# Performance work log

Hardware: AMD Instinct MI355X
Metric: run time of the kernel (lower is better)

## Reference

```python
import jax, jax.numpy as jnp
import numpy as np
from jax import lax

EPS = 1e-5
NUM_GROUPS = 32
OFFSET_SCALE = 1.0
K = 3            # deformable conv kernel size
KK = K * K
DWK = 7          # depthwise kernel size for offset predictor


def group_norm(x, gamma, beta, num_groups=NUM_GROUPS):
    B, C, H, W = x.shape
    xg = x.reshape(B, num_groups, C // num_groups, H, W)
    m = xg.mean(axis=(2, 3, 4), keepdims=True)
    v = xg.var(axis=(2, 3, 4), keepdims=True)
    xn = ((xg - m) * lax.rsqrt(v + EPS)).reshape(B, C, H, W)
    return xn * gamma[None, :, None, None] + beta[None, :, None, None]


def bilinear_gather(x, py, px):
    # x: [B,C,H,W]; py, px: [B,KK,H,W] absolute sample coords -> [B,C,KK,H,W]
    B, C, H, W = x.shape
    y0 = jnp.floor(py)
    x0 = jnp.floor(px)
    wy1 = py - y0
    wx1 = px - x0
    wy0 = 1.0 - wy1
    wx0 = 1.0 - wx1
    xf = x.reshape(B, C, H * W)

    def gather(yi, xi):
        valid = (yi >= 0) & (yi <= H - 1) & (xi >= 0) & (xi <= W - 1)
        yc = jnp.clip(yi, 0, H - 1).astype(jnp.int32)
        xc = jnp.clip(xi, 0, W - 1).astype(jnp.int32)
        idx = (yc * W + xc).reshape(B, -1)                      # [B, KK*H*W]
        g = jax.vmap(lambda a, i: a[:, i])(xf, idx)             # [B, C, KK*H*W]
        g = g.reshape(B, C, KK, H, W)
        return g * valid.astype(x.dtype)[:, None]

    out = (gather(y0, x0) * (wy0 * wx0)[:, None]
           + gather(y0, x0 + 1.0) * (wy0 * wx1)[:, None]
           + gather(y0 + 1.0, x0) * (wy1 * wx0)[:, None]
           + gather(y0 + 1.0, x0 + 1.0) * (wy1 * wx1)[:, None])
    return out


def deform_conv(x, dw, pw, pwb, w, b):
    # x: [B,C,H,W]; dw: [C,1,DWK,DWK] depthwise; pw: [2*KK,C,1,1]; w: [O,C,K,K]
    B, C, H, W = x.shape
    dn = ('NCHW', 'OIHW', 'NCHW')
    f = lax.conv_general_dilated(x, dw, (1, 1), 'SAME',
                                 feature_group_count=C, dimension_numbers=dn)
    off = lax.conv_general_dilated(f, pw, (1, 1), 'SAME', dimension_numbers=dn)
    off = (off + pwb[None, :, None, None]) * OFFSET_SCALE       # [B,2*KK,H,W]
    off = off.reshape(B, KK, 2, H, W)
    ks = jnp.arange(K, dtype=x.dtype) - (K - 1) / 2             # [-1,0,1]
    ky = jnp.repeat(ks, K)                                      # [KK]
    kx = jnp.tile(ks, K)
    yy, xx = jnp.meshgrid(jnp.arange(H, dtype=x.dtype),
                          jnp.arange(W, dtype=x.dtype), indexing='ij')
    py = yy[None, None] + ky[None, :, None, None] + off[:, :, 0]  # [B,KK,H,W]
    px = xx[None, None] + kx[None, :, None, None] + off[:, :, 1]
    sampled = bilinear_gather(x, py, px)                        # [B,C,KK,H,W]
    O = w.shape[0]
    out = jnp.einsum('bckhw,ock->bohw', sampled, w.reshape(O, C, KK))
    return out + b[None, :, None, None]


def setup_inputs() -> dict:
    key = jax.random.key(0)
    ks = jax.random.split(key, 10)
    B, C, H, W = 4, 256, 64, 64
    O = C
    x = jax.random.normal(ks[0], (B, C, H, W), dtype=jnp.float32)

    def conv_w(k, shape, fan_in):
        return jax.random.normal(k, shape, dtype=jnp.float32) / np.sqrt(fan_in)

    inp = {
        'x': x,
        'gn1_g': jnp.ones((C,), jnp.float32), 'gn1_b': jnp.zeros((C,), jnp.float32),
        'dw1': conv_w(ks[1], (C, 1, DWK, DWK), DWK * DWK),
        'pw1': jax.random.normal(ks[2], (2 * KK, C, 1, 1), jnp.float32) * 0.01,
        'pwb1': jnp.zeros((2 * KK,), jnp.float32),
        'w1': conv_w(ks[3], (O, C, K, K), C * KK),
        'b1': jnp.zeros((O,), jnp.float32),
        'gn2_g': jnp.ones((O,), jnp.float32), 'gn2_b': jnp.zeros((O,), jnp.float32),
        'dw2': conv_w(ks[4], (O, 1, DWK, DWK), DWK * DWK),
        'pw2': jax.random.normal(ks[5], (2 * KK, O, 1, 1), jnp.float32) * 0.01,
        'pwb2': jnp.zeros((2 * KK,), jnp.float32),
        'w2': conv_w(ks[6], (O, O, K, K), O * KK),
        'b2': jnp.zeros((O,), jnp.float32),
    }
    return inp


def reference(x, gn1_g, gn1_b, dw1, pw1, pwb1, w1, b1,
              gn2_g, gn2_b, dw2, pw2, pwb2, w2, b2):
    h = jax.nn.relu(group_norm(x, gn1_g, gn1_b))
    h = deform_conv(h, dw1, pw1, pwb1, w1, b1)
    h = jax.nn.relu(group_norm(h, gn2_g, gn2_b))
    # Dropout / DropPath are identity in eval mode
    h = deform_conv(h, dw2, pw2, pwb2, w2, b2)
    return h + x  # shortcut is Identity (in_channels == out_channels)
```

## Files before the change

### kernel.cpp

```cpp
#include <hip/hip_runtime.h>

#define B_    4
#define C_    256
#define H_    64
#define W_    64
#define HW_   4096
#define NG_   32
#define CPG_  8
#define KK_   9
#define NOFF_ 18

typedef __attribute__((ext_vector_type(8))) short short8;
typedef __attribute__((ext_vector_type(4))) short short4v;
typedef __attribute__((ext_vector_type(4))) float floatx4;

static __device__ __forceinline__ short f2bf(float f) {
    union { float f; unsigned u; } v; v.f = f;
    unsigned r = v.u + 0x7fff + ((v.u >> 16) & 1);
    return (short)(r >> 16);
}
static __device__ __forceinline__ float bf2f(short s) {
    union { unsigned u; float f; } v;
    v.u = ((unsigned)(unsigned short)s) << 16;
    return v.f;
}

__global__ __launch_bounds__(1024) void gn_relu_f32_kernel(
    const float* __restrict__ in, const float* __restrict__ gamma,
    const float* __restrict__ beta, short* __restrict__ outb)
{
    int b = blockIdx.x >> 5;
    int g = blockIdx.x & 31;
    const int N = CPG_ * HW_;
    size_t base = ((size_t)(b * C_ + g * CPG_)) * HW_;
    const float4* in4 = (const float4*)(in + base);
    int t = threadIdx.x;

    float s = 0.f, ss = 0.f;
    for (int i = t; i < N / 4; i += 1024) {
        float4 v = in4[i];
        s  += v.x + v.y + v.z + v.w;
        ss += v.x * v.x + v.y * v.y + v.z * v.z + v.w * v.w;
    }
    #pragma unroll
    for (int off = 32; off > 0; off >>= 1) {
        s  += __shfl_down(s, off, 64);
        ss += __shfl_down(ss, off, 64);
    }
    __shared__ float red[32];
    __shared__ float sh_rs, sh_m;
    int wid = t >> 6;
    if ((t & 63) == 0) { red[wid] = s; red[16 + wid] = ss; }
    __syncthreads();
    if (t == 0) {
        float S = 0.f, SS = 0.f;
        #pragma unroll
        for (int i = 0; i < 16; ++i) { S += red[i]; SS += red[16 + i]; }
        float m = S / (float)N;
        float var = SS / (float)N - m * m;
        sh_rs = rsqrtf(var + 1e-5f);
        sh_m = m;
    }
    __syncthreads();
    float rs = sh_rs, m = sh_m;
    short4v* out4 = (short4v*)(outb + base);
    for (int i = t; i < N / 4; i += 1024) {
        int ch = g * CPG_ + (i >> 10);
        float ga = gamma[ch] * rs;
        float be = beta[ch] - m * ga;
        float4 v = in4[i];
        short4v o;
        o.x = f2bf(fmaxf(fmaf(v.x, ga, be), 0.f));
        o.y = f2bf(fmaxf(fmaf(v.y, ga, be), 0.f));
        o.z = f2bf(fmaxf(fmaf(v.z, ga, be), 0.f));
        o.w = f2bf(fmaxf(fmaf(v.w, ga, be), 0.f));
        out4[i] = o;
    }
}

__global__ __launch_bounds__(1024) void gn_relu_bf16_kernel(
    const short* __restrict__ in, const float* __restrict__ gamma,
    const float* __restrict__ beta, short* __restrict__ outb)
{
    int b = blockIdx.x >> 5;
    int g = blockIdx.x & 31;
    const int N = CPG_ * HW_;
    size_t base = ((size_t)(b * C_ + g * CPG_)) * HW_;
    const short4v* in4 = (const short4v*)(in + base);
    int t = threadIdx.x;

    float s = 0.f, ss = 0.f;
    for (int i = t; i < N / 4; i += 1024) {
        short4v sv = in4[i];
        float vx = bf2f(sv.x), vy = bf2f(sv.y), vz = bf2f(sv.z), vw = bf2f(sv.w);
        s  += vx + vy + vz + vw;
        ss += vx * vx + vy * vy + vz * vz + vw * vw;
    }
    #pragma unroll
    for (int off = 32; off > 0; off >>= 1) {
        s  += __shfl_down(s, off, 64);
        ss += __shfl_down(ss, off, 64);
    }
    __shared__ float red[32];
    __shared__ float sh_rs, sh_m;
    int wid = t >> 6;
    if ((t & 63) == 0) { red[wid] = s; red[16 + wid] = ss; }
    __syncthreads();
    if (t == 0) {
        float S = 0.f, SS = 0.f;
        #pragma unroll
        for (int i = 0; i < 16; ++i) { S += red[i]; SS += red[16 + i]; }
        float m = S / (float)N;
        float var = SS / (float)N - m * m;
        sh_rs = rsqrtf(var + 1e-5f);
        sh_m = m;
    }
    __syncthreads();
    float rs = sh_rs, m = sh_m;
    short4v* out4 = (short4v*)(outb + base);
    for (int i = t; i < N / 4; i += 1024) {
        int ch = g * CPG_ + (i >> 10);
        float ga = gamma[ch] * rs;
        float be = beta[ch] - m * ga;
        short4v sv = in4[i];
        short4v o;
        o.x = f2bf(fmaxf(fmaf(bf2f(sv.x), ga, be), 0.f));
        o.y = f2bf(fmaxf(fmaf(bf2f(sv.y), ga, be), 0.f));
        o.z = f2bf(fmaxf(fmaf(bf2f(sv.z), ga, be), 0.f));
        o.w = f2bf(fmaxf(fmaf(bf2f(sv.w), ga, be), 0.f));
        out4[i] = o;
    }
}

__global__ __launch_bounds__(256) void dw7_kernel(
    const short* __restrict__ in, const float* __restrict__ dwk,
    short* __restrict__ out)
{
    int plane = blockIdx.x;
    int c = plane & (C_ - 1);
    const short* src = in + (size_t)plane * HW_;
    short* dst = out + (size_t)plane * HW_;
    __shared__ float tile[70 * 72];
    __shared__ float wk[49];
    int t = threadIdx.x;
    if (t < 49) wk[t] = dwk[c * 49 + t];
    for (int i = t; i < 70 * 72; i += 256) tile[i] = 0.f;
    __syncthreads();
    const short4v* src4 = (const short4v*)src;
    for (int i = t; i < HW_ / 4; i += 256) {
        short4v v = src4[i];
        int y = i >> 4, x = (i & 15) * 4;
        float* tp = &tile[(y + 3) * 72 + (x + 3)];
        tp[0] = bf2f(v.x); tp[1] = bf2f(v.y);
        tp[2] = bf2f(v.z); tp[3] = bf2f(v.w);
    }
    __syncthreads();
    #pragma unroll
    for (int it = 0; it < 4; ++it) {
        int idx = it * 256 + t;
        int y = idx >> 4;
        int x0 = (idx & 15) * 4;
        float a0 = 0.f, a1 = 0.f, a2 = 0.f, a3 = 0.f;
        #pragma unroll
        for (int dy = 0; dy < 7; ++dy) {
            const float* tr = &tile[(y + dy) * 72 + x0];
            float4 ra = *(const float4*)tr;
            float4 rb = *(const float4*)(tr + 4);
            float4 rc = *(const float4*)(tr + 8);
            float r[12] = {ra.x, ra.y, ra.z, ra.w,
                           rb.x, rb.y, rb.z, rb.w,
                           rc.x, rc.y, rc.z, rc.w};
            const float* wr = &wk[dy * 7];
            #pragma unroll
            for (int dx = 0; dx < 7; ++dx) {
                float wv = wr[dx];
                a0 = fmaf(r[dx], wv, a0);
                a1 = fmaf(r[dx + 1], wv, a1);
                a2 = fmaf(r[dx + 2], wv, a2);
                a3 = fmaf(r[dx + 3], wv, a3);
            }
        }
        short4v o;
        o.x = f2bf(a0); o.y = f2bf(a1); o.z = f2bf(a2); o.w = f2bf(a3);
        *(short4v*)&dst[y * 64 + x0] = o;
    }
}

__global__ __launch_bounds__(256) void transpose2_kernel(
    const short* __restrict__ srcA, short* __restrict__ dstA,
    const short* __restrict__ srcB, short* __restrict__ dstB)
{
    int blk = blockIdx.x;
    const short* src = (blk < 256) ? srcA : srcB;
    short*       dst = (blk < 256) ? dstA : dstB;
    int q = blk & 255;
    int b = q >> 6;
    int px0 = (q & 63) * 64;
    __shared__ unsigned ltile[64 * 132];
    int t = threadIdx.x;
    const short* sb = src + (size_t)b * C_ * HW_;

    int pq4 = t & 15, cphi = t >> 4;
    #pragma unroll
    for (int i = 0; i < 8; ++i) {
        int cp = i * 16 + cphi;
        const short* r0 = sb + (size_t)(2 * cp) * HW_ + px0 + pq4 * 4;
        short4v lo = *(const short4v*)r0;
        short4v hi = *(const short4v*)(r0 + HW_);
        #pragma unroll
        for (int j = 0; j < 4; ++j) {
            int pl = pq4 * 4 + j;
            unsigned wrd = (unsigned)(unsigned short)lo[j]
                         | ((unsigned)(unsigned short)hi[j] << 16);
            ltile[pl * 132 + (cp ^ ((pl & 7) << 2))] = wrd;
        }
    }
    __syncthreads();

    int co = t & 31, ph = t >> 5;
    #pragma unroll
    for (int r = 0; r < 8; ++r) {
        int pl = r * 8 + ph;
        uint4 v = *(const uint4*)&ltile[pl * 132 + ((co * 4) ^ ((pl & 7) << 2))];
        *(uint4*)(dst + ((size_t)b * HW_ + px0 + pl) * C_ + co * 8) = v;
    }
}

__global__ __launch_bounds__(256) void wpack_all_kernel(
    const float* __restrict__ w1, const float* __restrict__ w2,
    const float* __restrict__ pw1, const float* __restrict__ pw2,
    short* __restrict__ wp1, short* __restrict__ wp2,
    short* __restrict__ ppk1, short* __restrict__ ppk2)
{
    int blk = blockIdx.x;
    if (blk < 4608) {
        const float* w = (blk < 2304) ? w1 : w2;
        short* wp = (blk < 2304) ? wp1 : wp2;
        int idx = (blk % 2304) * 256 + threadIdx.x;
        int j    = idx & 7;
        int lane = (idx >> 3) & 63;
        int ot   = (idx >> 9) & 15;
        int slab = idx >> 13;
        int k = slab >> 3, cc = slab & 7;
        int o = ot * 16 + (lane & 15);
        int c = cc * 32 + (lane >> 4) * 8 + j;
        wp[idx] = f2bf(w[(size_t)(o * C_ + c) * KK_ + k]);
    } else {
        int q = blk - 4608;
        const float* pw = (q < 32) ? pw1 : pw2;
        short* ppk = (q < 32) ? ppk1 : ppk2;
        int idx = (q & 31) * 256 + threadIdx.x;
        int j = idx & 7, lane = (idx >> 3) & 63;
        int ot = (idx >> 9) & 1, sl = idx >> 10;
        int o = ot * 16 + (lane & 15);
        int k = sl * 32 + (lane >> 4) * 8 + j;
        ppk[idx] = (o < NOFF_) ? f2bf(pw[o * C_ + k]) : (short)0;
    }
}

__global__ __launch_bounds__(1024) void deform_fused_kernel(
    const short* __restrict__ ht,   const short* __restrict__ fdw,
    const short* __restrict__ ppk,  const float* __restrict__ pwb,
    const short* __restrict__ wp,   const float* __restrict__ bias,
    const float* __restrict__ resid, float* __restrict__ outf,
    short* __restrict__ outb)
{
    int b = blockIdx.x >> 6;
    int row = blockIdx.x & 63;
    __shared__ int   i00[576], i01[576], i10[576], i11[576];
    __shared__ float c00[576], c01[576], c10[576], c11[576];
    __shared__ float off_lds[NOFF_ * 64];
    __shared__ __align__(16) short sbuf[2][16384];
    int t = threadIdx.x;
    int wv = t >> 6, lane = t & 63;
    int pq = lane >> 4, pr = lane & 15;

    if (wv < 8) {
        int ot = wv & 1, ptw = wv >> 1;
        int px = ptw * 16 + pr;
        const short8* fb8 = (const short8*)(fdw +
            ((size_t)b * HW_ + row * 64 + px) * C_);
        const short8* ap = (const short8*)ppk;
        floatx4 pacc = (floatx4){0.f, 0.f, 0.f, 0.f};
        #pragma unroll
        for (int sl = 0; sl < 8; ++sl) {
            short8 af = ap[(sl * 2 + ot) * 64 + lane];
            short8 bf = fb8[sl * 4 + pq];
            pacc = __builtin_amdgcn_mfma_f32_16x16x32_bf16(af, bf, pacc, 0, 0, 0);
        }
        #pragma unroll
        for (int r = 0; r < 4; ++r) {
            int o = ot * 16 + pq * 4 + r;
            if (o < NOFF_) off_lds[o * 64 + px] = pacc[r] + pwb[o];
        }
    }
    __syncthreads();

    if (t < 576) {
        int e = t;
        int k = e >> 6, p = e & 63;
        float offy = off_lds[(2 * k) * 64 + p];
        float offx = off_lds[(2 * k + 1) * 64 + p];
        float py = (float)row + (float)(k / 3 - 1) + offy;
        float px = (float)p   + (float)(k % 3 - 1) + offx;
        float y0f = floorf(py), x0f = floorf(px);
        float wy1 = py - y0f, wx1 = px - x0f;
        float wy0 = 1.f - wy1, wx0 = 1.f - wx1;
        float y1f = y0f + 1.f, x1f = x0f + 1.f;
        bool vy0 = (y0f >= 0.f) && (y0f <= 63.f);
        bool vy1 = (y1f >= 0.f) && (y1f <= 63.f);
        bool vx0 = (x0f >= 0.f) && (x0f <= 63.f);
        bool vx1 = (x1f >= 0.f) && (x1f <= 63.f);
        int iy0 = (int)fminf(fmaxf(y0f, 0.f), 63.f);
        int iy1 = (int)fminf(fmaxf(y1f, 0.f), 63.f);
        int ix0 = (int)fminf(fmaxf(x0f, 0.f), 63.f);
        int ix1 = (int)fminf(fmaxf(x1f, 0.f), 63.f);
        i00[e] = iy0 * 64 + ix0; i01[e] = iy0 * 64 + ix1;
        i10[e] = iy1 * 64 + ix0; i11[e] = iy1 * 64 + ix1;
        c00[e] = (vy0 && vx0) ? wy0 * wx0 : 0.f;
        c01[e] = (vy0 && vx1) ? wy0 * wx1 : 0.f;
        c10[e] = (vy1 && vx0) ? wy1 * wx0 : 0.f;
        c11[e] = (vy1 && vx1) ? wy1 * wx1 : 0.f;
    }
    __syncthreads();

    int scb = t & 3, spx = (t >> 2) & 63, ssl0 = t >> 8;
    int u2 = spx * 4 + (scb ^ ((spx + (spx >> 2)) & 3));
    const short* hb = ht + ((size_t)b * HW_) * C_;
    const short* hb0 = hb + ssl0 * 32 + scb * 8;
    const short* hb1 = hb + (ssl0 + 4) * 32 + scb * 8;

    short8 ra[4], rb[4];
    auto prefetch = [&](int g) {
        int e = g * 64 + spx;
        int a00 = i00[e], a01 = i01[e], a10 = i10[e], a11 = i11[e];
        ra[0] = *(const short8*)(hb0 + (size_t)a00 * C_);
        ra[1] = *(const short8*)(hb0 + (size_t)a01 * C_);
        ra[2] = *(const short8*)(hb0 + (size_t)a10 * C_);
        ra[3] = *(const short8*)(hb0 + (size_t)a11 * C_);
        rb[0] = *(const short8*)(hb1 + (size_t)a00 * C_);
        rb[1] = *(const short8*)(hb1 + (size_t)a01 * C_);
        rb[2] = *(const short8*)(hb1 + (size_t)a10 * C_);
        rb[3] = *(const short8*)(hb1 + (size_t)a11 * C_);
    };
    auto stage_write = [&](int g, int bi) {
        int e = g * 64 + spx;
        float w00 = c00[e], w01 = c01[e], w10 = c10[e], w11 = c11[e];
        short8 va, vb;
        #pragma unroll
        for (int j = 0; j < 8; ++j) {
            va[j] = f2bf(w00 * bf2f(ra[0][j]) + w01 * bf2f(ra[1][j])
                       + w10 * bf2f(ra[2][j]) + w11 * bf2f(ra[3][j]));
            vb[j] = f2bf(w00 * bf2f(rb[0][j]) + w01 * bf2f(rb[1][j])
                       + w10 * bf2f(rb[2][j]) + w11 * bf2f(rb[3][j]));
        }
        *(short8*)&sbuf[bi][ssl0 * 2048 + u2 * 8] = va;
        *(short8*)&sbuf[bi][(ssl0 + 4) * 2048 + u2 * 8] = vb;
    };

    floatx4 acc[4];
    #pragma unroll
    for (int pt = 0; pt < 4; ++pt) acc[pt] = (floatx4){0.f, 0.f, 0.f, 0.f};
    int ub[4];
    #pragma unroll
    for (int pt = 0; pt < 4; ++pt) {
        int px2 = pt * 16 + pr;
        ub[pt] = px2 * 4 + (pq ^ ((px2 + (px2 >> 2)) & 3));
    }

    prefetch(0);
    stage_write(0, 0);
    prefetch(1);
    __syncthreads();

    const short8* wp8 = (const short8*)wp;
    for (int g = 0; g < 9; ++g) {
        const short* sb = sbuf[g & 1];
        #pragma unroll
        for (int half = 0; half < 2; ++half) {
            short8 af[4];
            #pragma unroll
            for (int q = 0; q < 4; ++q)
                af[q] = wp8[(size_t)((g * 8 + half * 4 + q) * 16 + wv) * 64 + lane];
            #pragma unroll
            for (int q = 0; q < 4; ++q) {
                int sl = half * 4 + q;
                #pragma unroll
                for (int pt = 0; pt < 4; ++pt) {
                    short8 bfv = *(const short8*)&sb[sl * 2048 + ub[pt] * 8];
                    acc[pt] = __builtin_amdgcn_mfma_f32_16x16x32_bf16(
                        af[q], bfv, acc[pt], 0, 0, 0);
                }
            }
        }
        if (g + 1 < 9) {
            stage_write(g + 1, (g + 1) & 1);
            if (g + 2 < 9) prefetch(g + 2);
        }
        __syncthreads();
    }

    #pragma unroll
    for (int r = 0; r < 4; ++r) {
        int o = wv * 16 + pq * 4 + r;
        float bo = bias[o];
        size_t obase = ((size_t)(b * C_ + o)) * HW_ + row * 64 + pr;
        #pragma unroll
        for (int pt = 0; pt < 4; ++pt) {
            float v = acc[pt][r] + bo;
            if (outf) {
                if (resid) v += resid[obase + pt * 16];
                outf[obase + pt * 16] = v;
            } else {
                outb[obase + pt * 16] = f2bf(v);
            }
        }
    }
}

extern "C" void kernel_launch(void* const* d_in, const int* in_sizes, int n_in,
                              void* d_out, int out_size, void* d_ws, size_t ws_size,
                              hipStream_t stream)
{
    const float* x     = (const float*)d_in[0];
    const float* gn1_g = (const float*)d_in[1];
    const float* gn1_b = (const float*)d_in[2];
    const float* dw1   = (const float*)d_in[3];
    const float* pw1   = (const float*)d_in[4];
    const float* pwb1  = (const float*)d_in[5];
    const float* w1    = (const float*)d_in[6];
    const float* b1    = (const float*)d_in[7];
    const float* gn2_g = (const float*)d_in[8];
    const float* gn2_b = (const float*)d_in[9];
    const float* dw2   = (const float*)d_in[10];
    const float* pw2   = (const float*)d_in[11];
    const float* pwb2  = (const float*)d_in[12];
    const float* w2    = (const float*)d_in[13];
    const float* b2    = (const float*)d_in[14];
    float* out = (float*)d_out;

    float* ws   = (float*)d_ws;
    short* y1b  = (short*)ws;
    short* hbf  = (short*)(ws + 2097152);
    short* hbt  = (short*)(ws + 4194304);
    short* fdwc = (short*)(ws + 6291456);
    short* fdwt = (short*)(ws + 8388608);
    short* wp1  = (short*)(ws + 10485760);
    short* wp2  = (short*)(ws + 10780672);
    short* ppk1 = (short*)(ws + 11075584);
    short* ppk2 = (short*)(ws + 11079680);

    wpack_all_kernel<<<4672, 256, 0, stream>>>(w1, w2, pw1, pw2,
                                               wp1, wp2, ppk1, ppk2);

    gn_relu_f32_kernel<<<B_ * NG_, 1024, 0, stream>>>(x, gn1_g, gn1_b, hbf);
    dw7_kernel<<<B_ * C_, 256, 0, stream>>>(hbf, dw1, fdwc);
    transpose2_kernel<<<512, 256, 0, stream>>>(hbf, hbt, fdwc, fdwt);
    deform_fused_kernel<<<B_ * H_, 1024, 0, stream>>>(
        hbt, fdwt, ppk1, pwb1, wp1, b1, nullptr, nullptr, y1b);

    gn_relu_bf16_kernel<<<B_ * NG_, 1024, 0, stream>>>(y1b, gn2_g, gn2_b, hbf);
    dw7_kernel<<<B_ * C_, 256, 0, stream>>>(hbf, dw2, fdwc);
    transpose2_kernel<<<512, 256, 0, stream>>>(hbf, hbt, fdwc, fdwt);
    deform_fused_kernel<<<B_ * H_, 1024, 0, stream>>>(
        hbt, fdwt, ppk2, pwb2, wp2, b2, x, out, nullptr);
}
```

Before: 251.0 us.

## Split deform conv over channel halves with 32x32 MFMA and atomic accumulation

The deformable conv kernel is restructured so each block handles half of the input channels (512 threads, twice as many blocks) and uses 32x32x16 bf16 MFMA tiles instead of 16x16x32, with the weight packing and the LDS swizzle re-laid out to match. The two channel-half partial sums are combined by float atomicAdd into a zeroed fp32 output, so the intermediate is now fp32 and the bf16 group-norm kernel is replaced by the fp32 one. Packed bf16 conversion via v_cvt_pk_bf16_f32 replaces scalar rounding in the staging blend. The change is meant to raise occupancy and MFMA efficiency. In exchange it adds two full-output memsets, atomic traffic, doubled bilinear index/weight setup, and nondeterministic summation order.

Measured after the change: 286.2 us. +14.0%, slower.

```diff
diff --git a/kernel.cpp b/kernel.cpp
--- a/kernel.cpp
+++ b/kernel.cpp
@@ -13,6 +13,7 @@
 typedef __attribute__((ext_vector_type(8))) short short8;
 typedef __attribute__((ext_vector_type(4))) short short4v;
 typedef __attribute__((ext_vector_type(4))) float floatx4;
+typedef __attribute__((ext_vector_type(16))) float floatx16;
 
 static __device__ __forceinline__ short f2bf(float f) {
     union { float f; unsigned u; } v; v.f = f;
@@ -23,6 +24,11 @@
     union { unsigned u; float f; } v;
     v.u = ((unsigned)(unsigned short)s) << 16;
     return v.f;
+}
+static __device__ __forceinline__ unsigned pkbf(float lo, float hi) {
+    unsigned r;
+    asm("v_cvt_pk_bf16_f32 %0, %1, %2" : "=v"(r) : "v"(lo), "v"(hi));
+    return r;
 }
 
 __global__ __launch_bounds__(1024) void gn_relu_f32_kernel(
@@ -74,60 +80,6 @@
         o.y = f2bf(fmaxf(fmaf(v.y, ga, be), 0.f));
         o.z = f2bf(fmaxf(fmaf(v.z, ga, be), 0.f));
         o.w = f2bf(fmaxf(fmaf(v.w, ga, be), 0.f));
-        out4[i] = o;
-    }
-}
-
-__global__ __launch_bounds__(1024) void gn_relu_bf16_kernel(
-    const short* __restrict__ in, const float* __restrict__ gamma,
-    const float* __restrict__ beta, short* __restrict__ outb)
-{
-    int b = blockIdx.x >> 5;
-    int g = blockIdx.x & 31;
-    const int N = CPG_ * HW_;
-    size_t base = ((size_t)(b * C_ + g * CPG_)) * HW_;
-    const short4v* in4 = (const short4v*)(in + base);
-    int t = threadIdx.x;
-
-    float s = 0.f, ss = 0.f;
-    for (int i = t; i < N / 4; i += 1024) {
-        short4v sv = in4[i];
-        float vx = bf2f(sv.x), vy = bf2f(sv.y), vz = bf2f(sv.z), vw = bf2f(sv.w);
-        s  += vx + vy + vz + vw;
-        ss += vx * vx + vy * vy + vz * vz + vw * vw;
-    }
-    #pragma unroll
-    for (int off = 32; off > 0; off >>= 1) {
-        s  += __shfl_down(s, off, 64);
-        ss += __shfl_down(ss, off, 64);
-    }
-    __shared__ float red[32];
-    __shared__ float sh_rs, sh_m;
-    int wid = t >> 6;
-    if ((t & 63) == 0) { red[wid] = s; red[16 + wid] = ss; }
-    __syncthreads();
-    if (t == 0) {
-        float S = 0.f, SS = 0.f;
-        #pragma unroll
-        for (int i = 0; i < 16; ++i) { S += red[i]; SS += red[16 + i]; }
-        float m = S / (float)N;
-        float var = SS / (float)N - m * m;
-        sh_rs = rsqrtf(var + 1e-5f);
-        sh_m = m;
-    }
-    __syncthreads();
-    float rs = sh_rs, m = sh_m;
-    short4v* out4 = (short4v*)(outb + base);
-    for (int i = t; i < N / 4; i += 1024) {
-        int ch = g * CPG_ + (i >> 10);
-        float ga = gamma[ch] * rs;
-        float be = beta[ch] - m * ga;
-        short4v sv = in4[i];
-        short4v o;
-        o.x = f2bf(fmaxf(fmaf(bf2f(sv.x), ga, be), 0.f));
-        o.y = f2bf(fmaxf(fmaf(bf2f(sv.y), ga, be), 0.f));
-        o.z = f2bf(fmaxf(fmaf(bf2f(sv.z), ga, be), 0.f));
-        o.w = f2bf(fmaxf(fmaf(bf2f(sv.w), ga, be), 0.f));
         out4[i] = o;
     }
 }
@@ -239,12 +191,12 @@
         int idx = (blk % 2304) * 256 + threadIdx.x;
         int j    = idx & 7;
         int lane = (idx >> 3) & 63;
-        int ot   = (idx >> 9) & 15;
-        int slab = idx >> 13;
-        int k = slab >> 3, cc = slab & 7;
-        int o = ot * 16 + (lane & 15);
-        int c = cc * 32 + (lane >> 4) * 8 + j;
-        wp[idx] = f2bf(w[(size_t)(o * C_ + c) * KK_ + k]);
+        int ot   = (idx >> 9) & 7;
+        int slab = idx >> 12;
+        int g = slab >> 4, cc16 = slab & 15;
+        int o = ot * 32 + (lane & 31);
+        int c = cc16 * 16 + (lane >> 5) * 8 + j;
+        wp[idx] = f2bf(w[(size_t)(o * C_ + c) * KK_ + g]);
     } else {
         int q = blk - 4608;
         const float* pw = (q < 32) ? pw1 : pw2;
@@ -258,24 +210,27 @@
     }
 }
 
-__global__ __launch_bounds__(1024) void deform_fused_kernel(
+__global__ __launch_bounds__(512, 4) void deform_fused_kernel(
     const short* __restrict__ ht,   const short* __restrict__ fdw,
     const short* __restrict__ ppk,  const float* __restrict__ pwb,
     const short* __restrict__ wp,   const float* __restrict__ bias,
-    const float* __restrict__ resid, float* __restrict__ outf,
-    short* __restrict__ outb)
-{
-    int b = blockIdx.x >> 6;
-    int row = blockIdx.x & 63;
+    const float* __restrict__ resid, float* __restrict__ outf)
+{
+    int blk = blockIdx.x;
+    int chalf = blk >> 8;
+    int qb = blk & 255;
+    int b = qb >> 6;
+    int row = qb & 63;
     __shared__ int   i00[576], i01[576], i10[576], i11[576];
     __shared__ float c00[576], c01[576], c10[576], c11[576];
-    __shared__ float off_lds[NOFF_ * 64];
-    __shared__ __align__(16) short sbuf[2][16384];
+    __shared__ __align__(16) short sbuf[2][8192];
+    float* off_lds = (float*)&sbuf[0][0];
     int t = threadIdx.x;
     int wv = t >> 6, lane = t & 63;
     int pq = lane >> 4, pr = lane & 15;
-
-    if (wv < 8) {
+    int l31 = lane & 31, hi = lane >> 5;
+
+    {
         int ot = wv & 1, ptw = wv >> 1;
         int px = ptw * 16 + pr;
         const short8* fb8 = (const short8*)(fdw +
@@ -296,8 +251,7 @@
     }
     __syncthreads();
 
-    if (t < 576) {
-        int e = t;
+    for (int e = t; e < 576; e += 512) {
         int k = e >> 6, p = e & 63;
         float offy = off_lds[(2 * k) * 64 + p];
         float offx = off_lds[(2 * k + 1) * 64 + p];
@@ -324,11 +278,14 @@
     }
     __syncthreads();
 
-    int scb = t & 3, spx = (t >> 2) & 63, ssl0 = t >> 8;
-    int u2 = spx * 4 + (scb ^ ((spx + (spx >> 2)) & 3));
-    const short* hb = ht + ((size_t)b * HW_) * C_;
-    const short* hb0 = hb + ssl0 * 32 + scb * 8;
-    const short* hb1 = hb + (ssl0 + 4) * 32 + scb * 8;
+    int c8a = t & 7;
+    int spx = t >> 3;
+    const short* hb = ht + ((size_t)b * HW_) * C_ + chalf * 128;
+    const short* hb0 = hb + c8a * 8;
+    const short* hb1 = hb + c8a * 8 + 64;
+    int slotA = (c8a ^ (spx & 15)) * 8;
+    int slotB = ((c8a + 8) ^ (spx & 15)) * 8;
+    int srow = spx * 128;
 
     short8 ra[4], rb[4];
     auto prefetch = [&](int g) {
@@ -346,27 +303,26 @@
     auto stage_write = [&](int g, int bi) {
         int e = g * 64 + spx;
         float w00 = c00[e], w01 = c01[e], w10 = c10[e], w11 = c11[e];
-        short8 va, vb;
-        #pragma unroll
-        for (int j = 0; j < 8; ++j) {
-            va[j] = f2bf(w00 * bf2f(ra[0][j]) + w01 * bf2f(ra[1][j])
-                       + w10 * bf2f(ra[2][j]) + w11 * bf2f(ra[3][j]));
-            vb[j] = f2bf(w00 * bf2f(rb[0][j]) + w01 * bf2f(rb[1][j])
-                       + w10 * bf2f(rb[2][j]) + w11 * bf2f(rb[3][j]));
-        }
-        *(short8*)&sbuf[bi][ssl0 * 2048 + u2 * 8] = va;
-        *(short8*)&sbuf[bi][(ssl0 + 4) * 2048 + u2 * 8] = vb;
+        uint4 va, vb;
+        float f0, f1;
+        #define BLEND(R, J) (w00 * bf2f(R[0][J]) + w01 * bf2f(R[1][J]) \
+                           + w10 * bf2f(R[2][J]) + w11 * bf2f(R[3][J]))
+        f0 = BLEND(ra, 0); f1 = BLEND(ra, 1); va.x = pkbf(f0, f1);
+        f0 = BLEND(ra, 2); f1 = BLEND(ra, 3); va.y = pkbf(f0, f1);
+        f0 = BLEND(ra, 4); f1 = BLEND(ra, 5); va.z = pkbf(f0, f1);
+        f0 = BLEND(ra, 6); f1 = BLEND(ra, 7); va.w = pkbf(f0, f1);
+        f0 = BLEND(rb, 0); f1 = BLEND(rb, 1); vb.x = pkbf(f0, f1);
+        f0 = BLEND(rb, 2); f1 = BLEND(rb, 3); vb.y = pkbf(f0, f1);
+        f0 = BLEND(rb, 4); f1 = BLEND(rb, 5); vb.z = pkbf(f0, f1);
+        f0 = BLEND(rb, 6); f1 = BLEND(rb, 7); vb.w = pkbf(f0, f1);
+        #undef BLEND
+        *(uint4*)&sbuf[bi][srow + slotA] = va;
+        *(uint4*)&sbuf[bi][srow + slotB] = vb;
     };
 
-    floatx4 acc[4];
-    #pragma unroll
-    for (int pt = 0; pt < 4; ++pt) acc[pt] = (floatx4){0.f, 0.f, 0.f, 0.f};
-    int ub[4];
-    #pragma unroll
-    for (int pt = 0; pt < 4; ++pt) {
-        int px2 = pt * 16 + pr;
-        ub[pt] = px2 * 4 + (pq ^ ((px2 + (px2 >> 2)) & 3));
-    }
+    floatx16 acc[2];
+    #pragma unroll
+    for (int i = 0; i < 16; ++i) { acc[0][i] = 0.f; acc[1][i] = 0.f; }
 
     prefetch(0);
     stage_write(0, 0);
@@ -374,23 +330,26 @@
     __syncthreads();
 
     const short8* wp8 = (const short8*)wp;
+    int base0 = l31 * 128;
+    int base1 = (32 + l31) * 128;
+    int msk = l31 & 15;
+
     for (int g = 0; g < 9; ++g) {
         const short* sb = sbuf[g & 1];
         #pragma unroll
-        for (int half = 0; half < 2; ++half) {
+        for (int kh = 0; kh < 2; ++kh) {
             short8 af[4];
             #pragma unroll
-            for (int q = 0; q < 4; ++q)
-                af[q] = wp8[(size_t)((g * 8 + half * 4 + q) * 16 + wv) * 64 + lane];
+            for (int qq = 0; qq < 4; ++qq)
+                af[qq] = wp8[(size_t)(((g * 16 + chalf * 8 + kh * 4 + qq) * 8 + wv) * 64 + lane)];
             #pragma unroll
-            for (int q = 0; q < 4; ++q) {
-                int sl = half * 4 + q;
-                #pragma unroll
-                for (int pt = 0; pt < 4; ++pt) {
-                    short8 bfv = *(const short8*)&sb[sl * 2048 + ub[pt] * 8];
-                    acc[pt] = __builtin_amdgcn_mfma_f32_16x16x32_bf16(
-                        af[q], bfv, acc[pt], 0, 0, 0);
-                }
+            for (int qq = 0; qq < 4; ++qq) {
+                int ks = kh * 4 + qq;
+                int so = ((((ks << 1) | hi) ^ msk) << 3);
+                short8 b0 = *(const short8*)&sb[base0 + so];
+                short8 b1 = *(const short8*)&sb[base1 + so];
+                acc[0] = __builtin_amdgcn_mfma_f32_32x32x16_bf16(af[qq], b0, acc[0], 0, 0, 0);
+                acc[1] = __builtin_amdgcn_mfma_f32_32x32x16_bf16(af[qq], b1, acc[1], 0, 0, 0);
             }
         }
         if (g + 1 < 9) {
@@ -401,20 +360,17 @@
     }
 
     #pragma unroll
-    for (int r = 0; r < 4; ++r) {
-        int o = wv * 16 + pq * 4 + r;
-        float bo = bias[o];
-        size_t obase = ((size_t)(b * C_ + o)) * HW_ + row * 64 + pr;
-        #pragma unroll
-        for (int pt = 0; pt < 4; ++pt) {
-            float v = acc[pt][r] + bo;
-            if (outf) {
-                if (resid) v += resid[obase + pt * 16];
-                outf[obase + pt * 16] = v;
-            } else {
-                outb[obase + pt * 16] = f2bf(v);
-            }
-        }
+    for (int r = 0; r < 16; ++r) {
+        int o = wv * 32 + (r & 3) + 8 * (r >> 2) + 4 * hi;
+        float v0 = acc[0][r], v1 = acc[1][r];
+        size_t ob = ((size_t)(b * C_ + o)) * HW_ + row * 64 + l31;
+        if (chalf == 0) {
+            float bo = bias[o];
+            v0 += bo; v1 += bo;
+            if (resid) { v0 += resid[ob]; v1 += resid[ob + 32]; }
+        }
+        atomicAdd(&outf[ob], v0);
+        atomicAdd(&outf[ob + 32], v1);
     }
 }
 
@@ -440,7 +396,6 @@
     float* out = (float*)d_out;
 
     float* ws   = (float*)d_ws;
-    short* y1b  = (short*)ws;
     short* hbf  = (short*)(ws + 2097152);
     short* hbt  = (short*)(ws + 4194304);
     short* fdwc = (short*)(ws + 6291456);
@@ -450,18 +405,22 @@
     short* ppk1 = (short*)(ws + 11075584);
     short* ppk2 = (short*)(ws + 11079680);
 
+    const size_t OUTBYTES = (size_t)B_ * C_ * HW_ * sizeof(float);
+
     wpack_all_kernel<<<4672, 256, 0, stream>>>(w1, w2, pw1, pw2,
                                                wp1, wp2, ppk1, ppk2);
 
+    hipMemsetAsync(d_out, 0, OUTBYTES, stream);
     gn_relu_f32_kernel<<<B_ * NG_, 1024, 0, stream>>>(x, gn1_g, gn1_b, hbf);
     dw7_kernel<<<B_ * C_, 256, 0, stream>>>(hbf, dw1, fdwc);
     transpose2_kernel<<<512, 256, 0, stream>>>(hbf, hbt, fdwc, fdwt);
-    deform_fused_kernel<<<B_ * H_, 1024, 0, stream>>>(
-        hbt, fdwt, ppk1, pwb1, wp1, b1, nullptr, nullptr, y1b);
-
-    gn_relu_bf16_kernel<<<B_ * NG_, 1024, 0, stream>>>(y1b, gn2_g, gn2_b, hbf);
+    deform_fused_kernel<<<512, 512, 0, stream>>>(
+        hbt, fdwt, ppk1, pwb1, wp1, b1, nullptr, out);
+
+    gn_relu_f32_kernel<<<B_ * NG_, 1024, 0, stream>>>(out, gn2_g, gn2_b, hbf);
     dw7_kernel<<<B_ * C_, 256, 0, stream>>>(hbf, dw2, fdwc);
     transpose2_kernel<<<512, 256, 0, stream>>>(hbf, hbt, fdwc, fdwt);
-    deform_fused_kernel<<<B_ * H_, 1024, 0, stream>>>(
-        hbt, fdwt, ppk2, pwb2, wp2, b2, x, out, nullptr);
-}
+    hipMemsetAsync(d_out, 0, OUTBYTES, stream);
+    deform_fused_kernel<<<512, 512, 0, stream>>>(
+        hbt, fdwt, ppk2, pwb2, wp2, b2, x, out);
+}
```

## Switch deform conv GEMM to 32x32x16 MFMA with split-K wave pairs

Applied to the files above, without the earlier changes.

Repacks the weights for 32x32 MFMA tiles and restructures the fused deformable conv main loop so each wave pair covers 32 output channels by 64 pixels, splitting the channel reduction across two waves. The partial sums are then combined through LDS. The staging buffer layout is changed to a per-half XOR-swizzled layout, and the bilinear blend packs results with v_cvt_pk_bf16_f32. Launch bounds request higher occupancy and the offset scratch now aliases sbuf to cut LDS use. The aim is fewer MFMA instructions and LDS reads per FLOP, at the cost of an extra reduction barrier and exchange through LDS.

Measured after the change: 249.1 us. About the same (-0.8%).

```diff
diff --git a/kernel.cpp b/kernel.cpp
--- a/kernel.cpp
+++ b/kernel.cpp
@@ -13,6 +13,7 @@
 typedef __attribute__((ext_vector_type(8))) short short8;
 typedef __attribute__((ext_vector_type(4))) short short4v;
 typedef __attribute__((ext_vector_type(4))) float floatx4;
+typedef __attribute__((ext_vector_type(16))) float floatx16;
 
 static __device__ __forceinline__ short f2bf(float f) {
     union { float f; unsigned u; } v; v.f = f;
@@ -23,6 +24,11 @@
     union { unsigned u; float f; } v;
     v.u = ((unsigned)(unsigned short)s) << 16;
     return v.f;
+}
+static __device__ __forceinline__ unsigned pkbf(float lo, float hi) {
+    unsigned r;
+    asm("v_cvt_pk_bf16_f32 %0, %1, %2" : "=v"(r) : "v"(lo), "v"(hi));
+    return r;
 }
 
 __global__ __launch_bounds__(1024) void gn_relu_f32_kernel(
@@ -239,12 +245,12 @@
         int idx = (blk % 2304) * 256 + threadIdx.x;
         int j    = idx & 7;
         int lane = (idx >> 3) & 63;
-        int ot   = (idx >> 9) & 15;
-        int slab = idx >> 13;
-        int k = slab >> 3, cc = slab & 7;
-        int o = ot * 16 + (lane & 15);
-        int c = cc * 32 + (lane >> 4) * 8 + j;
-        wp[idx] = f2bf(w[(size_t)(o * C_ + c) * KK_ + k]);
+        int ot   = (idx >> 9) & 7;
+        int slab = idx >> 12;
+        int g = slab >> 4, cc16 = slab & 15;
+        int o = ot * 32 + (lane & 31);
+        int c = cc16 * 16 + (lane >> 5) * 8 + j;
+        wp[idx] = f2bf(w[(size_t)(o * C_ + c) * KK_ + g]);
     } else {
         int q = blk - 4608;
         const float* pw = (q < 32) ? pw1 : pw2;
@@ -258,7 +264,7 @@
     }
 }
 
-__global__ __launch_bounds__(1024) void deform_fused_kernel(
+__global__ __launch_bounds__(1024, 4) void deform_fused_kernel(
     const short* __restrict__ ht,   const short* __restrict__ fdw,
     const short* __restrict__ ppk,  const float* __restrict__ pwb,
     const short* __restrict__ wp,   const float* __restrict__ bias,
@@ -269,11 +275,12 @@
     int row = blockIdx.x & 63;
     __shared__ int   i00[576], i01[576], i10[576], i11[576];
     __shared__ float c00[576], c01[576], c10[576], c11[576];
-    __shared__ float off_lds[NOFF_ * 64];
-    __shared__ __align__(16) short sbuf[2][16384];
+    __shared__ __align__(16) short sbuf[2][2][8192];
+    float* off_lds = (float*)&sbuf[0][0][0];
     int t = threadIdx.x;
     int wv = t >> 6, lane = t & 63;
     int pq = lane >> 4, pr = lane & 15;
+    int l31 = lane & 31, hi = lane >> 5;
 
     if (wv < 8) {
         int ot = wv & 1, ptw = wv >> 1;
@@ -324,11 +331,15 @@
     }
     __syncthreads();
 
-    int scb = t & 3, spx = (t >> 2) & 63, ssl0 = t >> 8;
-    int u2 = spx * 4 + (scb ^ ((spx + (spx >> 2)) & 3));
-    const short* hb = ht + ((size_t)b * HW_) * C_;
-    const short* hb0 = hb + ssl0 * 32 + scb * 8;
-    const short* hb1 = hb + (ssl0 + 4) * 32 + scb * 8;
+    int c8a = t & 7;
+    int pan = (t >> 3) & 1;
+    int spx = t >> 4;
+    const short* hb = ht + ((size_t)b * HW_) * C_ + pan * 128 + c8a * 8;
+    const short* hb0 = hb;
+    const short* hb1 = hb + 64;
+    int slotA = (c8a ^ (spx & 15)) * 8;
+    int slotB = ((c8a + 8) ^ (spx & 15)) * 8;
+    int srow = spx * 128;
 
     short8 ra[4], rb[4];
     auto prefetch = [&](int g) {
@@ -346,27 +357,30 @@
     auto stage_write = [&](int g, int bi) {
         int e = g * 64 + spx;
         float w00 = c00[e], w01 = c01[e], w10 = c10[e], w11 = c11[e];
-        short8 va, vb;
-        #pragma unroll
-        for (int j = 0; j < 8; ++j) {
-            va[j] = f2bf(w00 * bf2f(ra[0][j]) + w01 * bf2f(ra[1][j])
-                       + w10 * bf2f(ra[2][j]) + w11 * bf2f(ra[3][j]));
-            vb[j] = f2bf(w00 * bf2f(rb[0][j]) + w01 * bf2f(rb[1][j])
-                       + w10 * bf2f(rb[2][j]) + w11 * bf2f(rb[3][j]));
-        }
-        *(short8*)&sbuf[bi][ssl0 * 2048 + u2 * 8] = va;
-        *(short8*)&sbuf[bi][(ssl0 + 4) * 2048 + u2 * 8] = vb;
+        uint4 va, vb;
+        float f0, f1;
+        #define BLEND(R, J) (w00 * bf2f(R[0][J]) + w01 * bf2f(R[1][J]) \
+                           + w10 * bf2f(R[2][J]) + w11 * bf2f(R[3][J]))
+        f0 = BLEND(ra, 0); f1 = BLEND(ra, 1); va.x = pkbf(f0, f1);
+        f0 = BLEND(ra, 2); f1 = BLEND(ra, 3); va.y = pkbf(f0, f1);
+        f0 = BLEND(ra, 4); f1 = BLEND(ra, 5); va.z = pkbf(f0, f1);
+        f0 = BLEND(ra, 6); f1 = BLEND(ra, 7); va.w = pkbf(f0, f1);
+        f0 = BLEND(rb, 0); f1 = BLEND(rb, 1); vb.x = pkbf(f0, f1);
+        f0 = BLEND(rb, 2); f1 = BLEND(rb, 3); vb.y = pkbf(f0, f1);
+        f0 = BLEND(rb, 4); f1 = BLEND(rb, 5); vb.z = pkbf(f0, f1);
+        f0 = BLEND(rb, 6); f1 = BLEND(rb, 7); vb.w = pkbf(f0, f1);
+        #undef BLEND
+        short* sp = &sbuf[bi][pan][srow];
+        *(uint4*)&sp[slotA] = va;
+        *(uint4*)&sp[slotB] = vb;
     };
 
-    floatx4 acc[4];
-    #pragma unroll
-    for (int pt = 0; pt < 4; ++pt) acc[pt] = (floatx4){0.f, 0.f, 0.f, 0.f};
-    int ub[4];
-    #pragma unroll
-    for (int pt = 0; pt < 4; ++pt) {
-        int px2 = pt * 16 + pr;
-        ub[pt] = px2 * 4 + (pq ^ ((px2 + (px2 >> 2)) & 3));
-    }
+    int pairId = wv & 7;
+    int half = wv >> 3;
+
+    floatx16 acc[2];
+    #pragma unroll
+    for (int i = 0; i < 16; ++i) { acc[0][i] = 0.f; acc[1][i] = 0.f; }
 
     prefetch(0);
     stage_write(0, 0);
@@ -374,23 +388,24 @@
     __syncthreads();
 
     const short8* wp8 = (const short8*)wp;
+    int msk = l31 & 15;
+
     for (int g = 0; g < 9; ++g) {
-        const short* sb = sbuf[g & 1];
-        #pragma unroll
-        for (int half = 0; half < 2; ++half) {
+        const short* sb = &sbuf[g & 1][half][0];
+        #pragma unroll
+        for (int q4 = 0; q4 < 2; ++q4) {
             short8 af[4];
             #pragma unroll
-            for (int q = 0; q < 4; ++q)
-                af[q] = wp8[(size_t)((g * 8 + half * 4 + q) * 16 + wv) * 64 + lane];
+            for (int qq = 0; qq < 4; ++qq)
+                af[qq] = wp8[(size_t)(((g * 16 + half * 8 + q4 * 4 + qq) * 8 + pairId) * 64 + lane)];
             #pragma unroll
-            for (int q = 0; q < 4; ++q) {
-                int sl = half * 4 + q;
-                #pragma unroll
-                for (int pt = 0; pt < 4; ++pt) {
-                    short8 bfv = *(const short8*)&sb[sl * 2048 + ub[pt] * 8];
-                    acc[pt] = __builtin_amdgcn_mfma_f32_16x16x32_bf16(
-                        af[q], bfv, acc[pt], 0, 0, 0);
-                }
+            for (int qq = 0; qq < 4; ++qq) {
+                int ksl = q4 * 4 + qq;
+                int so = ((((ksl << 1) | hi) ^ msk) << 3);
+                short8 b0 = *(const short8*)&sb[l31 * 128 + so];
+                short8 b1 = *(const short8*)&sb[(32 + l31) * 128 + so];
+                acc[0] = __builtin_amdgcn_mfma_f32_32x32x16_bf16(af[qq], b0, acc[0], 0, 0, 0);
+                acc[1] = __builtin_amdgcn_mfma_f32_32x32x16_bf16(af[qq], b1, acc[1], 0, 0, 0);
             }
         }
         if (g + 1 < 9) {
@@ -400,20 +415,35 @@
         __syncthreads();
     }
 
-    #pragma unroll
-    for (int r = 0; r < 4; ++r) {
-        int o = wv * 16 + pq * 4 + r;
-        float bo = bias[o];
-        size_t obase = ((size_t)(b * C_ + o)) * HW_ + row * 64 + pr;
-        #pragma unroll
-        for (int pt = 0; pt < 4; ++pt) {
-            float v = acc[pt][r] + bo;
-            if (outf) {
-                if (resid) v += resid[obase + pt * 16];
-                outf[obase + pt * 16] = v;
-            } else {
-                outb[obase + pt * 16] = f2bf(v);
-            }
+    float* xch = (float*)&sbuf[0][0][0];
+    int wreg = (pairId * 2 + half) * 1024;
+    floatx16 aw = half ? acc[0] : acc[1];
+    floatx4* xq = (floatx4*)xch;
+    #pragma unroll
+    for (int j = 0; j < 4; ++j) {
+        floatx4 v = {aw[j * 4 + 0], aw[j * 4 + 1], aw[j * 4 + 2], aw[j * 4 + 3]};
+        xq[(wreg >> 2) + j * 64 + lane] = v;
+    }
+    __syncthreads();
+    int rreg = (pairId * 2 + (half ^ 1)) * 1024;
+    floatx16 ac = half ? acc[1] : acc[0];
+    #pragma unroll
+    for (int j = 0; j < 4; ++j) {
+        floatx4 v = xq[(rreg >> 2) + j * 64 + lane];
+        ac[j * 4 + 0] += v.x; ac[j * 4 + 1] += v.y;
+        ac[j * 4 + 2] += v.z; ac[j * 4 + 3] += v.w;
+    }
+
+    #pragma unroll
+    for (int r = 0; r < 16; ++r) {
+        int o = pairId * 32 + (r & 3) + 8 * (r >> 2) + 4 * hi;
+        float v = ac[r] + bias[o];
+        size_t ob = ((size_t)(b * C_ + o)) * HW_ + row * 64 + half * 32 + l31;
+        if (outf) {
+            if (resid) v += resid[ob];
+            outf[ob] = v;
+        } else {
+            outb[ob] = f2bf(v);
         }
     }
 }
```
